# Optimization experiments

Hardware: AMD Instinct MI355X
Metric: run time of the kernel (lower is better)

Reference implementation:

```python
import jax, jax.numpy as jnp
import numpy as np

ENCODER_DIM, DECODER_DIM, ATTENTION_DIM = 2048, 512, 512
B, L = 128, 196


def setup_inputs() -> dict:
    key = jax.random.key(0)
    ks = jax.random.split(key, 8)
    s_u = 1.0 / np.sqrt(ENCODER_DIM)
    s_w = 1.0 / np.sqrt(DECODER_DIM)
    s_a = 1.0 / np.sqrt(ATTENTION_DIM)
    return {
        "features": jax.random.normal(ks[0], (B, L, ENCODER_DIM), jnp.float32),
        "hidden_state": jax.random.normal(ks[1], (B, DECODER_DIM), jnp.float32),
        "U_w": jax.random.uniform(ks[2], (ENCODER_DIM, ATTENTION_DIM), jnp.float32, -s_u, s_u),
        "U_b": jax.random.uniform(ks[3], (ATTENTION_DIM,), jnp.float32, -s_u, s_u),
        "W_w": jax.random.uniform(ks[4], (DECODER_DIM, ATTENTION_DIM), jnp.float32, -s_w, s_w),
        "W_b": jax.random.uniform(ks[5], (ATTENTION_DIM,), jnp.float32, -s_w, s_w),
        "A_w": jax.random.uniform(ks[6], (ATTENTION_DIM,), jnp.float32, -s_a, s_a),
        "A_b": jax.random.uniform(ks[7], (1,), jnp.float32, -s_a, s_a),
    }


def reference(features, hidden_state, U_w, U_b, W_w, W_b, A_w, A_b):
    # u_hs: [B, L, A], w_ah: [B, A]
    u_hs = jnp.einsum('ble,ea->bla', features, U_w) + U_b
    w_ah = hidden_state @ W_w + W_b
    combined = jnp.tanh(u_hs + w_ah[:, None, :])          # [B, L, A]
    scores = jnp.einsum('bla,a->bl', combined, A_w) + A_b[0]  # [B, L]
    alpha = jax.nn.softmax(scores, axis=1)                 # [B, L]
    context = jnp.einsum('bl,ble->be', alpha, features)    # [B, E]
    return alpha, context
```

## Files before the change

### kernel.cpp

```cpp
#include <hip/hip_runtime.h>
#include <hip/hip_bf16.h>

#define ENC 2048
#define ADIM 512
#define DEC 512
#define NBATCH 128
#define NL 196
#define MTOT (NBATCH * NL)
#define NKT 32

typedef __attribute__((ext_vector_type(8))) short short8;
typedef __attribute__((ext_vector_type(4))) float f32x4;
typedef __attribute__((ext_vector_type(4))) unsigned int u32x4;

__device__ __forceinline__ unsigned short f2bf(float f) {
    __hip_bfloat16 h = __float2bfloat16(f);
    union { __hip_bfloat16 h; unsigned short u; } cv; cv.h = h; return cv.u;
}
__device__ __forceinline__ unsigned int f2bf2(float lo, float hi) {
    __hip_bfloat162 h = __float22bfloat162_rn(float2{lo, hi});
    union { __hip_bfloat162 h; unsigned int u; } cv; cv.h = h; return cv.u;
}

__device__ __forceinline__ void load_lds16(const void* g, void* l) {
    __builtin_amdgcn_global_load_lds(
        (const __attribute__((address_space(1))) unsigned int*)g,
        (__attribute__((address_space(3))) unsigned int*)l, 16, 0, 0);
}

__global__ void cvt_feat_kernel(const float* __restrict__ feat, unsigned short* __restrict__ featb) {
    const size_t total  = (size_t)MTOT * ENC;
    const size_t stride = (size_t)gridDim.x * blockDim.x * 8;
    size_t i = ((size_t)blockIdx.x * blockDim.x + threadIdx.x) * 8;
    for (; i < total; i += stride) {
        f32x4 lo = *(const f32x4*)(feat + i);
        f32x4 hi = *(const f32x4*)(feat + i + 4);
        u32x4 v;
        v.x = f2bf2(lo.x, lo.y); v.y = f2bf2(lo.z, lo.w);
        v.z = f2bf2(hi.x, hi.y); v.w = f2bf2(hi.z, hi.w);
        *(u32x4*)(featb + i) = v;
    }
}

__global__ void wah_kernel(const float* __restrict__ hidden, const float* __restrict__ Ww,
                           const float* __restrict__ Wb, float* __restrict__ wah) {
    __shared__ __align__(16) float hs[DEC];
    const int b = blockIdx.x, a = threadIdx.x;
    hs[a] = hidden[b * DEC + a];
    __syncthreads();
    float acc = Wb[a];
    #pragma unroll 4
    for (int d = 0; d < DEC; d += 4) {
        f32x4 h = *(const f32x4*)&hs[d];
        acc += h.x * Ww[(d    ) * ADIM + a];
        acc += h.y * Ww[(d + 1) * ADIM + a];
        acc += h.z * Ww[(d + 2) * ADIM + a];
        acc += h.w * Ww[(d + 3) * ADIM + a];
    }
    wah[b * ADIM + a] = acc;
}

__global__ void transpose_uw(const float* __restrict__ Uw, unsigned short* __restrict__ uwT) {
    __shared__ float t[32][33];
    const int k0 = blockIdx.x * 32, n0 = blockIdx.y * 32;
    const int tx = threadIdx.x, ty = threadIdx.y;
    #pragma unroll
    for (int i = 0; i < 4; ++i)
        t[ty + 8 * i][tx] = Uw[(size_t)(k0 + ty + 8 * i) * ADIM + n0 + tx];
    __syncthreads();
    #pragma unroll
    for (int i = 0; i < 4; ++i)
        uwT[(size_t)(n0 + ty + 8 * i) * ENC + k0 + tx] = f2bf(t[tx][ty + 8 * i]);
}

__global__ __launch_bounds__(256, 3) void gemm_score_bf16(
    const unsigned short* __restrict__ featb, const unsigned short* __restrict__ uwT,
    const float* __restrict__ Ub, const float* __restrict__ wahb,
    const float* __restrict__ Aw, float* __restrict__ part)
{
    __shared__ __align__(16) unsigned char As[16384];
    __shared__ __align__(16) unsigned char Bs[16384];

    const int tid  = threadIdx.x;
    const int lane = tid & 63;
    const int w    = tid >> 6;
    const int wr   = w >> 1, wc = w & 1;
    const int l15  = lane & 15, ldr = lane >> 4;

    const int bid  = blockIdx.x;
    const int work = (bid & 7) * 98 + (bid >> 3);
    const int mb   = work >> 2;
    const int nbk  = work & 3;

    const int swz = ((lane & 7) ^ ((lane >> 3) & 7)) << 3;
    const unsigned short* aS = featb + (size_t)(mb  * 128 + w * 32 + (lane >> 3)) * ENC + swz;
    const unsigned short* bS = uwT   + (size_t)(nbk * 128 + w * 32 + (lane >> 3)) * ENC + swz;

    int abyte[4][2], bbyte[4][2];
    #pragma unroll
    for (int f = 0; f < 4; ++f) {
        const int ra = wr * 64 + f * 16 + l15;
        const int rb = wc * 64 + f * 16 + l15;
        #pragma unroll
        for (int ks = 0; ks < 2; ++ks) {
            abyte[f][ks] = ra * 128 + (((ks * 4 + ldr) ^ (ra & 7)) << 4);
            bbyte[f][ks] = rb * 128 + (((ks * 4 + ldr) ^ (rb & 7)) << 4);
        }
    }

    f32x4 acc[4][4];
    #pragma unroll
    for (int i = 0; i < 4; ++i)
        #pragma unroll
        for (int j = 0; j < 4; ++j)
            acc[i][j] = (f32x4){0.f, 0.f, 0.f, 0.f};

    #pragma unroll 1
    for (int kt = 0; kt < NKT; ++kt) {
        #pragma unroll
        for (int c = 0; c < 4; ++c)
            load_lds16(aS + (size_t)kt * 64 + c * 8 * ENC, As + w * 4096 + c * 1024);
        #pragma unroll
        for (int c = 0; c < 4; ++c)
            load_lds16(bS + (size_t)kt * 64 + c * 8 * ENC, Bs + w * 4096 + c * 1024);
        __syncthreads();

        #pragma unroll
        for (int ks = 0; ks < 2; ++ks) {
            short8 af[4], bf[4];
            #pragma unroll
            for (int f = 0; f < 4; ++f) {
                af[f] = *(const short8*)(As + abyte[f][ks]);
                bf[f] = *(const short8*)(Bs + bbyte[f][ks]);
            }
            #pragma unroll
            for (int fm = 0; fm < 4; ++fm)
                #pragma unroll
                for (int fn = 0; fn < 4; ++fn)
                    acc[fm][fn] = __builtin_amdgcn_mfma_f32_16x16x32_bf16(
                        af[fm], bf[fn], acc[fm][fn], 0, 0, 0);
        }
        __syncthreads();
    }

    float ub4[4], aw4[4]; int cidx[4];
    #pragma unroll
    for (int f = 0; f < 4; ++f) {
        const int c = nbk * 128 + wc * 64 + f * 16 + l15;
        cidx[f] = c; ub4[f] = Ub[c]; aw4[f] = Aw[c];
    }
    #pragma unroll
    for (int fm = 0; fm < 4; ++fm) {
        #pragma unroll
        for (int r = 0; r < 4; ++r) {
            const int m = mb * 128 + wr * 64 + fm * 16 + ldr * 4 + r;
            const int b = m / NL;
            const float* wrow = wahb + b * ADIM;
            float s = 0.f;
            #pragma unroll
            for (int f = 0; f < 4; ++f)
                s += aw4[f] * tanhf(acc[fm][f][r] + ub4[f] + wrow[cidx[f]]);
            s += __shfl_xor(s, 1);
            s += __shfl_xor(s, 2);
            s += __shfl_xor(s, 4);
            s += __shfl_xor(s, 8);
            if (l15 == 0) part[(nbk * 2 + wc) * MTOT + m] = s;
        }
    }
}

__global__ __launch_bounds__(256, 4) void gemm_score_fp32(
    const float* __restrict__ feat, const unsigned short* __restrict__ uwT,
    const float* __restrict__ Ub, const float* __restrict__ wahb,
    const float* __restrict__ Aw, float* __restrict__ part)
{
    __shared__ __align__(16) unsigned char As[8192];
    __shared__ __align__(16) unsigned char Bs[16384];

    const int tid  = threadIdx.x;
    const int lane = tid & 63;
    const int w    = tid >> 6;
    const int l15  = lane & 15, ldr = lane >> 4;

    const int bid  = blockIdx.x;
    const int work = (bid & 7) * 196 + (bid >> 3);
    const int mb   = work >> 2;
    const int nbk  = work & 3;

    const int r_ = tid >> 2, kq = tid & 3;
    const float* aSrc = feat + (size_t)(mb * 64 + r_) * ENC + kq * 16;
    const int wA0 = r_ * 128 + (((kq * 2    ) ^ (r_ & 7)) << 4);
    const int wA1 = r_ * 128 + (((kq * 2 + 1) ^ (r_ & 7)) << 4);

    const unsigned short* bSrc = uwT
        + (size_t)(nbk * 128 + w * 32 + (lane >> 3)) * ENC
        + (((lane & 7) ^ ((lane >> 3) & 7)) << 3);

    int abyte[4][2], bbyte[2][2];
    #pragma unroll
    for (int ks = 0; ks < 2; ++ks) {
        const int sl = ((ks * 4 + ldr) ^ (l15 & 7)) << 4;
        #pragma unroll
        for (int f = 0; f < 4; ++f)
            abyte[f][ks] = (f * 16 + l15) * 128 + sl;
        #pragma unroll
        for (int g = 0; g < 2; ++g)
            bbyte[g][ks] = (w * 32 + g * 16 + l15) * 128 + sl;
    }

    f32x4 acc[4][2];
    #pragma unroll
    for (int i = 0; i < 4; ++i)
        #pragma unroll
        for (int j = 0; j < 2; ++j)
            acc[i][j] = (f32x4){0.f, 0.f, 0.f, 0.f};

    #pragma unroll 1
    for (int kt = 0; kt < NKT; ++kt) {
        const f32x4* p = (const f32x4*)(aSrc + (size_t)kt * 64);
        f32x4 a0 = p[0], a1 = p[1], a2 = p[2], a3 = p[3];
        #pragma unroll
        for (int c = 0; c < 4; ++c)
            load_lds16(bSrc + (size_t)kt * 64 + c * 8 * ENC, Bs + w * 4096 + c * 1024);
        u32x4 w0, w1;
        w0.x = f2bf2(a0.x, a0.y); w0.y = f2bf2(a0.z, a0.w);
        w0.z = f2bf2(a1.x, a1.y); w0.w = f2bf2(a1.z, a1.w);
        w1.x = f2bf2(a2.x, a2.y); w1.y = f2bf2(a2.z, a2.w);
        w1.z = f2bf2(a3.x, a3.y); w1.w = f2bf2(a3.z, a3.w);
        *(u32x4*)(As + wA0) = w0;
        *(u32x4*)(As + wA1) = w1;
        __syncthreads();

        #pragma unroll
        for (int ks = 0; ks < 2; ++ks) {
            short8 af[4], bf[2];
            #pragma unroll
            for (int f = 0; f < 4; ++f) af[f] = *(const short8*)(As + abyte[f][ks]);
            #pragma unroll
            for (int g = 0; g < 2; ++g) bf[g] = *(const short8*)(Bs + bbyte[g][ks]);
            #pragma unroll
            for (int fm = 0; fm < 4; ++fm)
                #pragma unroll
                for (int g = 0; g < 2; ++g)
                    acc[fm][g] = __builtin_amdgcn_mfma_f32_16x16x32_bf16(
                        af[fm], bf[g], acc[fm][g], 0, 0, 0);
        }
        __syncthreads();
    }

    float ub2[2], aw2[2]; int cidx[2];
    #pragma unroll
    for (int g = 0; g < 2; ++g) {
        const int c = nbk * 128 + w * 32 + g * 16 + l15;
        cidx[g] = c; ub2[g] = Ub[c]; aw2[g] = Aw[c];
    }
    #pragma unroll
    for (int fm = 0; fm < 4; ++fm) {
        #pragma unroll
        for (int r = 0; r < 4; ++r) {
            const int m = mb * 64 + fm * 16 + ldr * 4 + r;
            const int b = m / NL;
            const float* wrow = wahb + b * ADIM;
            #pragma unroll
            for (int g = 0; g < 2; ++g) {
                float s = aw2[g] * tanhf(acc[fm][g][r] + ub2[g] + wrow[cidx[g]]);
                s += __shfl_xor(s, 1);
                s += __shfl_xor(s, 2);
                s += __shfl_xor(s, 4);
                s += __shfl_xor(s, 8);
                if (l15 == 0) part[(nbk * 8 + w * 2 + g) * MTOT + m] = s;
            }
        }
    }
}

__global__ void softmax_kernel(const float* __restrict__ part, const float* __restrict__ Ab,
                               float* __restrict__ alpha, int npart) {
    const int b = blockIdx.x, t = threadIdx.x;
    float sv = 0.f;
    if (t < NL) {
        sv = Ab[0];
        for (int p = 0; p < npart; ++p) sv += part[p * MTOT + b * NL + t];
    }
    float v = (t < NL) ? sv : -3.4e38f;
    #pragma unroll
    for (int o = 32; o >= 1; o >>= 1) v = fmaxf(v, __shfl_xor(v, o));
    __shared__ float rm[4], rs[4];
    if ((t & 63) == 0) rm[t >> 6] = v;
    __syncthreads();
    const float bm = fmaxf(fmaxf(rm[0], rm[1]), fmaxf(rm[2], rm[3]));
    const float e = (t < NL) ? expf(sv - bm) : 0.f;
    float s = e;
    #pragma unroll
    for (int o = 32; o >= 1; o >>= 1) s += __shfl_xor(s, o);
    if ((t & 63) == 0) rs[t >> 6] = s;
    __syncthreads();
    const float bs = rs[0] + rs[1] + rs[2] + rs[3];
    if (t < NL) alpha[b * NL + t] = e / bs;
}

__global__ void context_kernel(const float* __restrict__ feat, const float* __restrict__ alpha,
                               float* __restrict__ ctx) {
    __shared__ float al[NL];
    const int b = blockIdx.x, chunk = blockIdx.y, t = threadIdx.x;
    for (int i = t; i < NL; i += 128) al[i] = alpha[b * NL + i];
    __syncthreads();
    const int e0 = chunk * 512 + t * 4;
    const float* fp = feat + (size_t)b * NL * ENC + e0;
    f32x4 acc0 = (f32x4){0.f, 0.f, 0.f, 0.f};
    f32x4 acc1 = (f32x4){0.f, 0.f, 0.f, 0.f};
    #pragma unroll 2
    for (int l = 0; l < NL; l += 2) {
        f32x4 f0 = *(const f32x4*)(fp + (size_t)l * ENC);
        f32x4 f1 = *(const f32x4*)(fp + (size_t)(l + 1) * ENC);
        acc0 += al[l] * f0;
        acc1 += al[l + 1] * f1;
    }
    f32x4 rsum = acc0 + acc1;
    *(f32x4*)(ctx + (size_t)b * ENC + e0) = rsum;
}

extern "C" void kernel_launch(void* const* d_in, const int* in_sizes, int n_in,
                              void* d_out, int out_size, void* d_ws, size_t ws_size,
                              hipStream_t stream) {
    const float* feat   = (const float*)d_in[0];
    const float* hidden = (const float*)d_in[1];
    const float* Uw     = (const float*)d_in[2];
    const float* Ub     = (const float*)d_in[3];
    const float* Ww     = (const float*)d_in[4];
    const float* Wb     = (const float*)d_in[5];
    const float* Aw     = (const float*)d_in[6];
    const float* Ab     = (const float*)d_in[7];

    float* out   = (float*)d_out;
    float* alpha = out;
    float* ctx   = out + MTOT;

    const size_t FEATB_BYTES = (size_t)MTOT * ENC * 2;
    const size_t SMALL_NEED  = 262144 + 2097152 + (size_t)32 * MTOT * 4;
    const size_t BIG_NEED    = FEATB_BYTES + 262144 + 2097152 + (size_t)8 * MTOT * 4;

    char* ws = (char*)d_ws;

    if (ws_size >= BIG_NEED) {
        unsigned short* featb = (unsigned short*)ws;
        float*          wahb  = (float*)(ws + FEATB_BYTES);
        unsigned short* uwT   = (unsigned short*)(ws + FEATB_BYTES + 262144);
        float*          partb = (float*)(ws + FEATB_BYTES + 262144 + 2097152);

        cvt_feat_kernel<<<dim3(2048), dim3(256), 0, stream>>>(feat, featb);
        wah_kernel<<<dim3(128), dim3(512), 0, stream>>>(hidden, Ww, Wb, wahb);
        transpose_uw<<<dim3(64, 16), dim3(32, 8), 0, stream>>>(Uw, uwT);
        gemm_score_bf16<<<dim3(784), dim3(256), 0, stream>>>(featb, uwT, Ub, wahb, Aw, partb);
        softmax_kernel<<<dim3(128), dim3(256), 0, stream>>>(partb, Ab, alpha, 8);
        context_kernel<<<dim3(128, 4), dim3(128), 0, stream>>>(feat, alpha, ctx);
    } else {
        float*          wahb  = (float*)ws;
        unsigned short* uwT   = (unsigned short*)(ws + 262144);
        float*          partb = (float*)(ws + 262144 + 2097152);
        (void)SMALL_NEED;

        wah_kernel<<<dim3(128), dim3(512), 0, stream>>>(hidden, Ww, Wb, wahb);
        transpose_uw<<<dim3(64, 16), dim3(32, 8), 0, stream>>>(Uw, uwT);
        gemm_score_fp32<<<dim3(1568), dim3(256), 0, stream>>>(feat, uwT, Ub, wahb, Aw, partb);
        softmax_kernel<<<dim3(128), dim3(256), 0, stream>>>(partb, Ab, alpha, 32);
        context_kernel<<<dim3(128, 4), dim3(128), 0, stream>>>(feat, alpha, ctx);
    }
}
```

Baseline: 196.8 us.

## Stream GEMM B operand from registers with double-buffered prefetch; context from bf16 copy

The bf16 GEMM now loads the U weight tile straight from global memory into registers, double-buffered across k-steps, instead of staging it through LDS. This halves LDS use and overlaps the next B fetch with the current MFMAs, with raised wave priority during compute. The context reduction now reads the bf16 copy of the features instead of fp32, which halves its memory traffic but lowers precision of the context output. Register pressure rises from holding 16 short8 B fragments.

```diff
diff --git a/kernel.cpp b/kernel.cpp
--- a/kernel.cpp
+++ b/kernel.cpp
@@ -20,6 +20,9 @@
 __device__ __forceinline__ unsigned int f2bf2(float lo, float hi) {
     __hip_bfloat162 h = __float22bfloat162_rn(float2{lo, hi});
     union { __hip_bfloat162 h; unsigned int u; } cv; cv.h = h; return cv.u;
+}
+__device__ __forceinline__ float bf2f(unsigned short u) {
+    union { unsigned int u; float f; } cv; cv.u = ((unsigned int)u) << 16; return cv.f;
 }
 
 __device__ __forceinline__ void load_lds16(const void* g, void* l) {
@@ -79,7 +82,6 @@
     const float* __restrict__ Aw, float* __restrict__ part)
 {
     __shared__ __align__(16) unsigned char As[16384];
-    __shared__ __align__(16) unsigned char Bs[16384];
 
     const int tid  = threadIdx.x;
     const int lane = tid & 63;
@@ -93,19 +95,17 @@
     const int nbk  = work & 3;
 
     const int swz = ((lane & 7) ^ ((lane >> 3) & 7)) << 3;
-    const unsigned short* aS = featb + (size_t)(mb  * 128 + w * 32 + (lane >> 3)) * ENC + swz;
-    const unsigned short* bS = uwT   + (size_t)(nbk * 128 + w * 32 + (lane >> 3)) * ENC + swz;
-
-    int abyte[4][2], bbyte[4][2];
+    const unsigned short* aS = featb + (size_t)(mb * 128 + w * 32 + (lane >> 3)) * ENC + swz;
+
+    const unsigned short* bBase = uwT + (size_t)(nbk * 128 + wc * 64 + l15) * ENC + ldr * 8;
+
+    int abyte[4][2];
     #pragma unroll
     for (int f = 0; f < 4; ++f) {
         const int ra = wr * 64 + f * 16 + l15;
-        const int rb = wc * 64 + f * 16 + l15;
-        #pragma unroll
-        for (int ks = 0; ks < 2; ++ks) {
+        #pragma unroll
+        for (int ks = 0; ks < 2; ++ks)
             abyte[f][ks] = ra * 128 + (((ks * 4 + ldr) ^ (ra & 7)) << 4);
-            bbyte[f][ks] = rb * 128 + (((ks * 4 + ldr) ^ (rb & 7)) << 4);
-        }
     }
 
     f32x4 acc[4][4];
@@ -115,33 +115,78 @@
         for (int j = 0; j < 4; ++j)
             acc[i][j] = (f32x4){0.f, 0.f, 0.f, 0.f};
 
+    short8 be0, be1, be2, be3, be4, be5, be6, be7;
+    short8 bo0, bo1, bo2, bo3, bo4, bo5, bo6, bo7;
+
+#define DMA_A(KTI) {                                                          \
+    _Pragma("unroll")                                                         \
+    for (int c = 0; c < 4; ++c)                                               \
+        load_lds16(aS + (size_t)(KTI) * 64 + c * 8 * ENC,                     \
+                   As + w * 4096 + c * 1024);                                 \
+}
+#define ISSUE_B(KTI, B0, B1, B2, B3, B4, B5, B6, B7) {                        \
+    const unsigned short* bp = bBase + (size_t)(KTI) * 64;                    \
+    B0 = *(const short8*)(bp + 0 * 16 * ENC +  0);                            \
+    B1 = *(const short8*)(bp + 0 * 16 * ENC + 32);                            \
+    B2 = *(const short8*)(bp + 1 * 16 * ENC +  0);                            \
+    B3 = *(const short8*)(bp + 1 * 16 * ENC + 32);                            \
+    B4 = *(const short8*)(bp + 2 * 16 * ENC +  0);                            \
+    B5 = *(const short8*)(bp + 2 * 16 * ENC + 32);                            \
+    B6 = *(const short8*)(bp + 3 * 16 * ENC +  0);                            \
+    B7 = *(const short8*)(bp + 3 * 16 * ENC + 32);                            \
+    __builtin_amdgcn_sched_barrier(0);                                        \
+}
+#define COMPUTE(B0, B1, B2, B3, B4, B5, B6, B7) {                             \
+    __builtin_amdgcn_s_setprio(1);                                            \
+    {                                                                         \
+        short8 af[4];                                                         \
+        _Pragma("unroll")                                                     \
+        for (int f = 0; f < 4; ++f) af[f] = *(const short8*)(As + abyte[f][0]); \
+        _Pragma("unroll")                                                     \
+        for (int fm = 0; fm < 4; ++fm) {                                      \
+            acc[fm][0] = __builtin_amdgcn_mfma_f32_16x16x32_bf16(af[fm], B0, acc[fm][0], 0, 0, 0); \
+            acc[fm][1] = __builtin_amdgcn_mfma_f32_16x16x32_bf16(af[fm], B2, acc[fm][1], 0, 0, 0); \
+            acc[fm][2] = __builtin_amdgcn_mfma_f32_16x16x32_bf16(af[fm], B4, acc[fm][2], 0, 0, 0); \
+            acc[fm][3] = __builtin_amdgcn_mfma_f32_16x16x32_bf16(af[fm], B6, acc[fm][3], 0, 0, 0); \
+        }                                                                     \
+    }                                                                         \
+    {                                                                         \
+        short8 af[4];                                                         \
+        _Pragma("unroll")                                                     \
+        for (int f = 0; f < 4; ++f) af[f] = *(const short8*)(As + abyte[f][1]); \
+        _Pragma("unroll")                                                     \
+        for (int fm = 0; fm < 4; ++fm) {                                      \
+            acc[fm][0] = __builtin_amdgcn_mfma_f32_16x16x32_bf16(af[fm], B1, acc[fm][0], 0, 0, 0); \
+            acc[fm][1] = __builtin_amdgcn_mfma_f32_16x16x32_bf16(af[fm], B3, acc[fm][1], 0, 0, 0); \
+            acc[fm][2] = __builtin_amdgcn_mfma_f32_16x16x32_bf16(af[fm], B5, acc[fm][2], 0, 0, 0); \
+            acc[fm][3] = __builtin_amdgcn_mfma_f32_16x16x32_bf16(af[fm], B7, acc[fm][3], 0, 0, 0); \
+        }                                                                     \
+    }                                                                         \
+    __builtin_amdgcn_s_setprio(0);                                            \
+}
+
+    DMA_A(0);
+    ISSUE_B(0, be0, be1, be2, be3, be4, be5, be6, be7);
+    __syncthreads();
+
     #pragma unroll 1
-    for (int kt = 0; kt < NKT; ++kt) {
-        #pragma unroll
-        for (int c = 0; c < 4; ++c)
-            load_lds16(aS + (size_t)kt * 64 + c * 8 * ENC, As + w * 4096 + c * 1024);
-        #pragma unroll
-        for (int c = 0; c < 4; ++c)
-            load_lds16(bS + (size_t)kt * 64 + c * 8 * ENC, Bs + w * 4096 + c * 1024);
+    for (int kt = 0; kt < NKT; kt += 2) {
+        const int k1 = (kt + 1 < NKT) ? kt + 1 : NKT - 1;
+        const int k2 = (kt + 2 < NKT) ? kt + 2 : NKT - 1;
+        ISSUE_B(k1, bo0, bo1, bo2, bo3, bo4, bo5, bo6, bo7);
+        COMPUTE(be0, be1, be2, be3, be4, be5, be6, be7);
+        __builtin_amdgcn_s_barrier();
+        DMA_A(k1);
         __syncthreads();
-
-        #pragma unroll
-        for (int ks = 0; ks < 2; ++ks) {
-            short8 af[4], bf[4];
-            #pragma unroll
-            for (int f = 0; f < 4; ++f) {
-                af[f] = *(const short8*)(As + abyte[f][ks]);
-                bf[f] = *(const short8*)(Bs + bbyte[f][ks]);
-            }
-            #pragma unroll
-            for (int fm = 0; fm < 4; ++fm)
-                #pragma unroll
-                for (int fn = 0; fn < 4; ++fn)
-                    acc[fm][fn] = __builtin_amdgcn_mfma_f32_16x16x32_bf16(
-                        af[fm], bf[fn], acc[fm][fn], 0, 0, 0);
-        }
+        ISSUE_B(k2, be0, be1, be2, be3, be4, be5, be6, be7);
+        COMPUTE(bo0, bo1, bo2, bo3, bo4, bo5, bo6, bo7);
+        __builtin_amdgcn_s_barrier();
+        DMA_A(k2);
         __syncthreads();
     }
+#undef DMA_A
+#undef ISSUE_B
+#undef COMPUTE
 
     float ub4[4], aw4[4]; int cidx[4];
     #pragma unroll
@@ -299,6 +344,34 @@
     if (t < NL) alpha[b * NL + t] = e / bs;
 }
 
+__global__ void context_bf16_kernel(const unsigned short* __restrict__ featb,
+                                    const float* __restrict__ alpha, float* __restrict__ ctx) {
+    __shared__ float al[NL];
+    const int b = blockIdx.x, chunk = blockIdx.y, t = threadIdx.x;
+    for (int i = t; i < NL; i += 128) al[i] = alpha[b * NL + i];
+    __syncthreads();
+    const int e0 = chunk * 1024 + t * 8;
+    const unsigned short* fp = featb + (size_t)b * NL * ENC + e0;
+    float a0=0.f,a1=0.f,a2=0.f,a3=0.f,a4=0.f,a5=0.f,a6=0.f,a7=0.f;
+    for (int l = 0; l < NL; ++l) {
+        short8 v = *(const short8*)(fp + (size_t)l * ENC);
+        const float sc = al[l];
+        a0 += sc * bf2f((unsigned short)v[0]);
+        a1 += sc * bf2f((unsigned short)v[1]);
+        a2 += sc * bf2f((unsigned short)v[2]);
+        a3 += sc * bf2f((unsigned short)v[3]);
+        a4 += sc * bf2f((unsigned short)v[4]);
+        a5 += sc * bf2f((unsigned short)v[5]);
+        a6 += sc * bf2f((unsigned short)v[6]);
+        a7 += sc * bf2f((unsigned short)v[7]);
+    }
+    float* cp = ctx + (size_t)b * ENC + e0;
+    f32x4 r0 = (f32x4){a0, a1, a2, a3};
+    f32x4 r1 = (f32x4){a4, a5, a6, a7};
+    *(f32x4*)cp = r0;
+    *(f32x4*)(cp + 4) = r1;
+}
+
 __global__ void context_kernel(const float* __restrict__ feat, const float* __restrict__ alpha,
                                float* __restrict__ ctx) {
     __shared__ float al[NL];
@@ -337,7 +410,6 @@
     float* ctx   = out + MTOT;
 
     const size_t FEATB_BYTES = (size_t)MTOT * ENC * 2;
-    const size_t SMALL_NEED  = 262144 + 2097152 + (size_t)32 * MTOT * 4;
     const size_t BIG_NEED    = FEATB_BYTES + 262144 + 2097152 + (size_t)8 * MTOT * 4;
 
     char* ws = (char*)d_ws;
@@ -353,12 +425,11 @@
         transpose_uw<<<dim3(64, 16), dim3(32, 8), 0, stream>>>(Uw, uwT);
         gemm_score_bf16<<<dim3(784), dim3(256), 0, stream>>>(featb, uwT, Ub, wahb, Aw, partb);
         softmax_kernel<<<dim3(128), dim3(256), 0, stream>>>(partb, Ab, alpha, 8);
-        context_kernel<<<dim3(128, 4), dim3(128), 0, stream>>>(feat, alpha, ctx);
+        context_bf16_kernel<<<dim3(128, 2), dim3(128), 0, stream>>>(featb, alpha, ctx);
     } else {
         float*          wahb  = (float*)ws;
         unsigned short* uwT   = (unsigned short*)(ws + 262144);
         float*          partb = (float*)(ws + 262144 + 2097152);
-        (void)SMALL_NEED;
 
         wah_kernel<<<dim3(128), dim3(512), 0, stream>>>(hidden, Ww, Wb, wahb);
         transpose_uw<<<dim3(64, 16), dim3(32, 8), 0, stream>>>(Uw, uwT);
```

After: 252.9 us. +28.5%, slower.
